# Performance work log

Hardware: AMD Instinct MI355X
Metric: run time of the kernel (lower is better)

## Reference

```python
import jax, jax.numpy as jnp
import numpy as np

N = 50000      # nodes
E = 800000     # edges (avg degree 16)
IN = 128       # input feature dim
HID = 32       # per-head hidden dim
H = 4          # attention heads
C = 40         # num classes
SLOPE = 0.2    # leaky relu negative slope


def setup_inputs() -> dict:
    key = jax.random.key(0)
    ks = jax.random.split(key, 14)
    s = 0.05
    inputs = jax.random.normal(ks[0], (N, IN), jnp.float32)
    target = jax.random.normal(ks[1], (N, IN), jnp.float32)
    lamb = jax.random.uniform(ks[2], (1,), jnp.float32)
    src = jax.random.randint(ks[3], (E,), 0, N, jnp.int32)
    dst = jax.random.randint(ks[4], (E,), 0, N, jnp.int32)
    W0 = jax.random.normal(ks[5], (IN, H * HID), jnp.float32) * s
    al0 = jax.random.normal(ks[6], (H, HID), jnp.float32) * s
    ar0 = jax.random.normal(ks[7], (H, HID), jnp.float32) * s
    W1 = jax.random.normal(ks[8], (H * HID, H * HID), jnp.float32) * s
    al1 = jax.random.normal(ks[9], (H, HID), jnp.float32) * s
    ar1 = jax.random.normal(ks[10], (H, HID), jnp.float32) * s
    Wout = jax.random.normal(ks[11], (H * HID, C), jnp.float32) * s
    bout = jnp.zeros((C,), jnp.float32)
    return dict(inputs=inputs, target=target, lamb=lamb,
                W0=W0, al0=al0, ar0=ar0, W1=W1, al1=al1, ar1=ar1,
                Wout=Wout, bout=bout, src=src, dst=dst)


def gat_conv(h, W, al, ar, src, dst, residual):
    # h: [N, in_dim]; W: [in_dim, H*HID]; al/ar: [H, HID]
    feat = (h @ W).reshape(N, H, HID)                  # [N,H,D]
    el = jnp.einsum('nhd,hd->nh', feat, al)            # [N,H]
    er = jnp.einsum('nhd,hd->nh', feat, ar)            # [N,H]
    e = jax.nn.leaky_relu(el[src] + er[dst], SLOPE)    # [E,H]
    # edge softmax over incoming edges of each dst node
    emax = jax.ops.segment_max(e, dst, num_segments=N)  # [N,H]
    ee = jnp.exp(e - emax[dst])                          # [E,H]
    denom = jax.ops.segment_sum(ee, dst, num_segments=N)
    a = ee / denom[dst]                                  # [E,H]
    msg = feat[src] * a[:, :, None]                      # [E,H,D]
    out = jax.ops.segment_sum(msg, dst, num_segments=N)  # [N,H,D]
    if residual:
        out = out + h.reshape(N, H, HID)  # identity residual (in == H*HID)
    return jax.nn.elu(out)


def reference(inputs, target, lamb, W0, al0, ar0, W1, al1, ar1, Wout, bout, src, dst):
    def path(x):
        h = gat_conv(x, W0, al0, ar0, src, dst, residual=False).reshape(N, H * HID)
        h = gat_conv(h, W1, al1, ar1, src, dst, residual=True).reshape(N, H * HID)
        return h

    h = path(inputs)
    h2 = path(target)
    lam = lamb[0]
    h = lam * h + (1.0 - lam) * h2   # mixup_hidden=True
    logits = h @ Wout + bout
    return (h, logits)
```

## Files before the change

### kernel.cpp

```cpp
#include <hip/hip_runtime.h>
#include <hip/hip_bf16.h>
#include <cstddef>

#define GN 50000
#define GE 800000
#define GH 4
#define GD 32
#define SLOPE 0.2f
#define LOG2E 1.4426950408889634f

typedef unsigned short ushort_t;
typedef unsigned int uint_t;
using short8 = __attribute__((ext_vector_type(8))) short;
using float4v = __attribute__((ext_vector_type(4))) float;

__device__ __forceinline__ ushort_t f2bf(float f) {
    union { float f; uint_t u; } v; v.f = f;
    uint_t r = v.u + 0x7fff + ((v.u >> 16) & 1);
    return (ushort_t)(r >> 16);
}
__device__ __forceinline__ float bflo(uint_t u) { return __uint_as_float(u << 16); }
__device__ __forceinline__ float bfhi(uint_t u) { return __uint_as_float(u & 0xffff0000u); }
__device__ __forceinline__ float bfu(ushort_t u) { return __uint_as_float((uint_t)u << 16); }

__device__ __forceinline__ uint_t cvt_pk_bf16(float lo, float hi) {
    uint_t r;
    asm("v_cvt_pk_bf16_f32 %0, %1, %2" : "=v"(r) : "v"(lo), "v"(hi));
    return r;
}

#if __has_builtin(__builtin_amdgcn_exp2f)
#define EXP2F(x) __builtin_amdgcn_exp2f(x)
#else
#define EXP2F(x) exp2f(x)
#endif

#define SWZ_B(v, imm) __uint_as_float((uint_t)__builtin_amdgcn_ds_swizzle((int)__float_as_uint(v), (imm)))

__device__ __forceinline__ int slotmap(int a) {
    return (a < GN) ? (a << 1) : (((a - GN) << 1) | 1);
}

#define NEXT 144
#define WSTRIDE (NEXT * 128)

__global__ __launch_bounds__(256) void k_cvt_hist(
    const float* __restrict__ W0, const float* __restrict__ W1,
    const float* __restrict__ Wout,
    const float* __restrict__ al0, const float* __restrict__ ar0,
    const float* __restrict__ al1, const float* __restrict__ ar1,
    ushort_t* __restrict__ wbt, ushort_t* __restrict__ woutb,
    const int* __restrict__ dst, int* __restrict__ deg, int* __restrict__ rank,
    int cvtb, int E) {
    if ((int)blockIdx.x >= cvtb) {
        int i = ((blockIdx.x - cvtb) * 256 + threadIdx.x) * 4;
        if (i + 3 < E) {
            int4 d = *(const int4*)&dst[i];
            rank[i + 0] = atomicAdd(&deg[d.x], 1);
            rank[i + 1] = atomicAdd(&deg[d.y], 1);
            rank[i + 2] = atomicAdd(&deg[d.z], 1);
            rank[i + 3] = atomicAdd(&deg[d.w], 1);
        } else {
            for (int k = i; k < E; k++) rank[k] = atomicAdd(&deg[dst[k]], 1);
        }
        return;
    }
    int t = blockIdx.x * 256 + threadIdx.x;
    if (t < 2 * WSTRIDE) {
        int m = t / WSTRIDE;
        int o = t % WSTRIDE;
        int n = o >> 7, k = o & 127;
        const float* W = m ? W1 : W0;
        float v;
        if (n < 128) {
            v = W[k * 128 + n];
        } else if (n < 136) {
            int j = n - 128;
            int h = j & 3;
            const float* a = (j < 4) ? (m ? al1 : al0) : (m ? ar1 : ar0);
            float s = 0.f;
#pragma unroll 8
            for (int d = 0; d < 32; d++) s += W[k * 128 + h * 32 + d] * a[h * 32 + d];
            v = s * LOG2E;
        } else {
            v = 0.f;
        }
        wbt[t] = f2bf(v);
    } else {
        int u = t - 2 * WSTRIDE;
        if (u < 48 * 128) {
            int n = u >> 7, k = u & 127;
            float w = (n < 40) ? Wout[k * 40 + n] : 0.f;
            ushort_t h = f2bf(w);
            woutb[u] = h;
            woutb[48 * 128 + u] = f2bf(w - bfu(h));
        }
    }
}

__global__ void k_scan1(const int* __restrict__ deg, int* __restrict__ row_ptr,
                        int* __restrict__ partials, int n) {
    __shared__ int s[256];
    int t = threadIdx.x;
    int i = blockIdx.x * 256 + t;
    int v = (i < n) ? deg[i] : 0;
    s[t] = v;
    __syncthreads();
    for (int off = 1; off < 256; off <<= 1) {
        int add = (t >= off) ? s[t - off] : 0;
        __syncthreads();
        s[t] += add;
        __syncthreads();
    }
    if (i < n) row_ptr[i] = s[t] - v;
    if (t == 255) partials[blockIdx.x] = s[255];
}

__global__ void k_scan2(int* __restrict__ partials, int nb) {
    __shared__ int s[256];
    int t = threadIdx.x;
    int v = (t < nb) ? partials[t] : 0;
    s[t] = v;
    __syncthreads();
    for (int off = 1; off < 256; off <<= 1) {
        int add = (t >= off) ? s[t - off] : 0;
        __syncthreads();
        s[t] += add;
        __syncthreads();
    }
    if (t < nb) partials[t] = s[t] - v;
}

__global__ void k_scan3(int* __restrict__ row_ptr,
                        const int* __restrict__ partials, int n, int E) {
    int i = blockIdx.x * 256 + threadIdx.x;
    if (i < n) {
        row_ptr[i] += partials[i >> 8];
        if (i == 0) row_ptr[n] = E;
    }
}

__global__ void k_fill(const int* __restrict__ src, const int* __restrict__ dst,
                       const int* __restrict__ rank, const int* __restrict__ row_ptr,
                       int* __restrict__ csr_src, int E) {
    int i = (blockIdx.x * 256 + threadIdx.x) * 4;
    if (i + 3 < E) {
        int4 d = *(const int4*)&dst[i];
        int4 s = *(const int4*)&src[i];
        int4 r = *(const int4*)&rank[i];
        csr_src[row_ptr[d.x] + r.x] = s.x;
        csr_src[row_ptr[d.y] + r.y] = s.y;
        csr_src[row_ptr[d.z] + r.z] = s.z;
        csr_src[row_ptr[d.w] + r.w] = s.w;
    } else {
        for (int k = i; k < E; k++)
            csr_src[row_ptr[dst[k]] + rank[k]] = src[k];
    }
}

__device__ __forceinline__ void store_c_ext(ushort_t* __restrict__ Cb,
                                            float* __restrict__ el,
                                            float* __restrict__ er,
                                            const float4v acc[2][9],
                                            int r0, int quad, int col, int M) {
#pragma unroll
    for (int rt = 0; rt < 2; rt++)
#pragma unroll
        for (int nt = 0; nt < 8; nt++) {
            int rb = r0 + rt * 16 + quad * 4;
            int c = nt * 16 + col;
            uint_t p01 = cvt_pk_bf16(acc[rt][nt][0], acc[rt][nt][1]);
            uint_t p23 = cvt_pk_bf16(acc[rt][nt][2], acc[rt][nt][3]);
            if (rb + 0 < M) Cb[(size_t)slotmap(rb + 0) * 128 + c] = (ushort_t)p01;
            if (rb + 1 < M) Cb[(size_t)slotmap(rb + 1) * 128 + c] = (ushort_t)(p01 >> 16);
            if (rb + 2 < M) Cb[(size_t)slotmap(rb + 2) * 128 + c] = (ushort_t)p23;
            if (rb + 3 < M) Cb[(size_t)slotmap(rb + 3) * 128 + c] = (ushort_t)(p23 >> 16);
        }
    if (col < 8) {
        float* dstp = (col < 4) ? el : er;
        int h = col & 3;
#pragma unroll
        for (int rt = 0; rt < 2; rt++)
#pragma unroll
            for (int r = 0; r < 4; r++) {
                int row = r0 + rt * 16 + quad * 4 + r;
                if (row < M) dstp[slotmap(row) * 4 + h] = acc[rt][8][r];
            }
    }
}

__global__ __launch_bounds__(256) void gemm_mfma32(const float* __restrict__ A0,
                                                   const float* __restrict__ A1,
                                                   const ushort_t* __restrict__ WbT,
                                                   ushort_t* __restrict__ Cb,
                                                   float* __restrict__ el,
                                                   float* __restrict__ er, int M) {
    __shared__ ushort_t Bs[NEXT][136];
    int tid = threadIdx.x;
    for (int i = tid; i < NEXT * 16; i += 256) {
        int n = i >> 4;
        int kc = (i & 15) << 3;
        *(short8*)&Bs[n][kc] = *(const short8*)&WbT[n * 128 + kc];
    }
    __syncthreads();
    int wid = tid >> 6, lane = tid & 63;
    int r0 = blockIdx.x * 128 + wid * 32;
    int col = lane & 15, quad = lane >> 4;
    float4v acc[2][9];
#pragma unroll
    for (int rt = 0; rt < 2; rt++)
#pragma unroll
        for (int t = 0; t < 9; t++) acc[rt][t] = (float4v){0.f, 0.f, 0.f, 0.f};
    int ar_[2] = {r0 + col, r0 + 16 + col};
    const float* Ap[2];
#pragma unroll
    for (int rt = 0; rt < 2; rt++) {
        int a = ar_[rt];
        Ap[rt] = (a < M) ? ((a < GN) ? (A0 + (size_t)a * 128)
                                     : (A1 + (size_t)(a - GN) * 128)) : nullptr;
    }
#pragma unroll
    for (int ks = 0; ks < 4; ks++) {
        short8 af[2];
#pragma unroll
        for (int rt = 0; rt < 2; rt++) {
            af[rt] = (short8){};
            if (Ap[rt]) {
                float4 v0 = *(const float4*)&Ap[rt][ks * 32 + quad * 8];
                float4 v1 = *(const float4*)&Ap[rt][ks * 32 + quad * 8 + 4];
                union { short8 s; uint_t u[4]; } cv;
                cv.u[0] = cvt_pk_bf16(v0.x, v0.y);
                cv.u[1] = cvt_pk_bf16(v0.z, v0.w);
                cv.u[2] = cvt_pk_bf16(v1.x, v1.y);
                cv.u[3] = cvt_pk_bf16(v1.z, v1.w);
                af[rt] = cv.s;
            }
        }
#pragma unroll
        for (int nt = 0; nt < 9; nt++) {
            short8 bf = *(const short8*)&Bs[nt * 16 + col][ks * 32 + quad * 8];
            acc[0][nt] = __builtin_amdgcn_mfma_f32_16x16x32_bf16(af[0], bf, acc[0][nt], 0, 0, 0);
            acc[1][nt] = __builtin_amdgcn_mfma_f32_16x16x32_bf16(af[1], bf, acc[1][nt], 0, 0, 0);
        }
    }
    store_c_ext(Cb, el, er, acc, r0, quad, col, M);
}

__global__ __launch_bounds__(256) void gemm_mfma(const ushort_t* __restrict__ A,
                                                 const ushort_t* __restrict__ WbT,
                                                 ushort_t* __restrict__ Cb,
                                                 float* __restrict__ el,
                                                 float* __restrict__ er, int M) {
    __shared__ ushort_t Bs[NEXT][136];
    int tid = threadIdx.x;
    for (int i = tid; i < NEXT * 16; i += 256) {
        int n = i >> 4;
        int kc = (i & 15) << 3;
        *(short8*)&Bs[n][kc] = *(const short8*)&WbT[n * 128 + kc];
    }
    __syncthreads();
    int wid = tid >> 6, lane = tid & 63;
    int r0 = blockIdx.x * 128 + wid * 32;
    int col = lane & 15, quad = lane >> 4;
    float4v acc[2][9];
#pragma unroll
    for (int rt = 0; rt < 2; rt++)
#pragma unroll
        for (int t = 0; t < 9; t++) acc[rt][t] = (float4v){0.f, 0.f, 0.f, 0.f};
    int ar_[2] = {r0 + col, r0 + 16 + col};
    const ushort_t* Ap[2];
#pragma unroll
    for (int rt = 0; rt < 2; rt++) {
        int a = ar_[rt];
        Ap[rt] = (a < M) ? (A + (size_t)slotmap(a) * 128) : nullptr;
    }
#pragma unroll
    for (int ks = 0; ks < 4; ks++) {
        short8 af[2];
#pragma unroll
        for (int rt = 0; rt < 2; rt++) {
            af[rt] = (short8){};
            if (Ap[rt]) af[rt] = *(const short8*)&Ap[rt][ks * 32 + quad * 8];
        }
#pragma unroll
        for (int nt = 0; nt < 9; nt++) {
            short8 bf = *(const short8*)&Bs[nt * 16 + col][ks * 32 + quad * 8];
            acc[0][nt] = __builtin_amdgcn_mfma_f32_16x16x32_bf16(af[0], bf, acc[0][nt], 0, 0, 0);
            acc[1][nt] = __builtin_amdgcn_mfma_f32_16x16x32_bf16(af[1], bf, acc[1][nt], 0, 0, 0);
        }
    }
    store_c_ext(Cb, el, er, acc, r0, quad, col, M);
}

__device__ __forceinline__ void agg_core(
    const ushort_t* __restrict__ featb, const float* __restrict__ el, float ern,
    const int* __restrict__ csr_src, int base, int deg, uint_t eo, uint_t fofs,
    int lk, float& v0, float& v1, float& v2, float& v3) {
    if (deg <= 0) { v0 = v1 = v2 = v3 = 0.f; return; }
    float a0 = 0.f, a1 = 0.f, a2 = 0.f, a3 = 0.f, ss = 0.f;
    int nblk = (deg + 15) >> 4;
    int e1 = base + deg - 1;
    int jb = base;
    int s[16], t[16];
#pragma unroll
    for (int k = 0; k < 16; k++) s[k] = csr_src[min(jb + k, e1)];
    float elA = el[(uint_t)csr_src[min(jb + lk, e1)] * 8u + eo];
    float elB = el[(uint_t)csr_src[min(jb + lk + 8, e1)] * 8u + eo];
    for (int b = 0;;) {
        int rem = deg - (b << 4);
        uint2 f[16];
#pragma unroll
        for (int k = 0; k < 16; k++)
            f[k] = *(const uint2*)&featb[(uint_t)s[k] * 256u + fofs];
        bool more = (b + 1) < nblk;
        float elA2 = 0.f, elB2 = 0.f;
        if (more) {
            int nj = jb + 16;
#pragma unroll
            for (int k = 0; k < 16; k++) t[k] = csr_src[min(nj + k, e1)];
            elA2 = el[(uint_t)csr_src[min(nj + lk, e1)] * 8u + eo];
            elB2 = el[(uint_t)csr_src[min(nj + lk + 8, e1)] * 8u + eo];
        }
        float eA = elA + ern; eA = fmaxf(eA, SLOPE * eA);
        float eB = elB + ern; eB = fmaxf(eB, SLOPE * eB);
        float wA = (lk < rem) ? EXP2F(eA) : 0.f;
        float wB = (lk + 8 < rem) ? EXP2F(eB) : 0.f;
        float wv[16];
        wv[0]  = SWZ_B(wA, 0x018); wv[1]  = SWZ_B(wA, 0x038);
        wv[2]  = SWZ_B(wA, 0x058); wv[3]  = SWZ_B(wA, 0x078);
        wv[4]  = SWZ_B(wA, 0x098); wv[5]  = SWZ_B(wA, 0x0B8);
        wv[6]  = SWZ_B(wA, 0x0D8); wv[7]  = SWZ_B(wA, 0x0F8);
        wv[8]  = SWZ_B(wB, 0x018); wv[9]  = SWZ_B(wB, 0x038);
        wv[10] = SWZ_B(wB, 0x058); wv[11] = SWZ_B(wB, 0x078);
        wv[12] = SWZ_B(wB, 0x098); wv[13] = SWZ_B(wB, 0x0B8);
        wv[14] = SWZ_B(wB, 0x0D8); wv[15] = SWZ_B(wB, 0x0F8);
#pragma unroll
        for (int k = 0; k < 16; k++) {
            float w = wv[k];
            ss += w;
            a0 += w * bflo(f[k].x);
            a1 += w * bfhi(f[k].x);
            a2 += w * bflo(f[k].y);
            a3 += w * bfhi(f[k].y);
        }
        if (!more) break;
        b++; jb += 16;
#pragma unroll
        for (int k = 0; k < 16; k++) s[k] = t[k];
        elA = elA2; elB = elB2;
    }
    float inv = 1.f / ss;
    v0 = a0 * inv; v1 = a1 * inv; v2 = a2 * inv; v3 = a3 * inv;
}

__global__ __launch_bounds__(512) void gat_agg_l1(
    const ushort_t* __restrict__ featb, const float* __restrict__ el,
    const float* __restrict__ er, const int* __restrict__ row_ptr,
    const int* __restrict__ csr_src, ushort_t* __restrict__ abuf) {
    int n = __builtin_amdgcn_readfirstlane(blockIdx.x * 8 + (threadIdx.x >> 6));
    if (n >= GN) return;
    int lane = threadIdx.x & 63;
    int half = lane >> 5;
    int q = lane & 31;
    int lk = lane & 7, q4 = q << 2;
    uint_t eo = (uint_t)(half * 4 + ((lane >> 3) & 3));
    uint_t fofs = (uint_t)(half * 128 + q4);
    float ern = er[(uint_t)n * 8u + eo];
    int base = row_ptr[n];
    int deg = row_ptr[n + 1] - base;
    float v0, v1, v2, v3;
    agg_core(featb, el, ern, csr_src, base, deg, eo, fofs, lk, v0, v1, v2, v3);
    v0 = v0 > 0.f ? v0 : __expf(v0) - 1.f;
    v1 = v1 > 0.f ? v1 : __expf(v1) - 1.f;
    v2 = v2 > 0.f ? v2 : __expf(v2) - 1.f;
    v3 = v3 > 0.f ? v3 : __expf(v3) - 1.f;
    size_t idx = ((size_t)(2 * n + half)) * 128 + q4;
    uint2 o;
    o.x = cvt_pk_bf16(v0, v1);
    o.y = cvt_pk_bf16(v2, v3);
    *(uint2*)&abuf[idx] = o;
}

__global__ __launch_bounds__(512) void gat_agg_l2(
    const ushort_t* __restrict__ featb, const float* __restrict__ el,
    const float* __restrict__ er, const int* __restrict__ row_ptr,
    const int* __restrict__ csr_src, const ushort_t* __restrict__ resid,
    const float* __restrict__ lamb, float* __restrict__ outh) {
    int tid = threadIdx.x;
    int n = __builtin_amdgcn_readfirstlane(blockIdx.x * 8 + (tid >> 6));
    if (n >= GN) return;
    int lane = tid & 63;
    int half = lane >> 5;
    int q = lane & 31;
    int lk = lane & 7, q4 = q << 2;
    uint_t eo = (uint_t)(half * 4 + ((lane >> 3) & 3));
    uint_t fofs = (uint_t)(half * 128 + q4);
    float ern = er[(uint_t)n * 8u + eo];
    int base = row_ptr[n];
    int deg = row_ptr[n + 1] - base;
    float v0, v1, v2, v3;
    agg_core(featb, el, ern, csr_src, base, deg, eo, fofs, lk, v0, v1, v2, v3);
    size_t idx = ((size_t)(2 * n + half)) * 128 + q4;
    ushort4 r = *(const ushort4*)&resid[idx];
    v0 += bfu(r.x); v1 += bfu(r.y); v2 += bfu(r.z); v3 += bfu(r.w);
    v0 = v0 > 0.f ? v0 : __expf(v0) - 1.f;
    v1 = v1 > 0.f ? v1 : __expf(v1) - 1.f;
    v2 = v2 > 0.f ? v2 : __expf(v2) - 1.f;
    v3 = v3 > 0.f ? v3 : __expf(v3) - 1.f;
    float p0 = __shfl_xor(v0, 32, 64);
    float p1 = __shfl_xor(v1, 32, 64);
    float p2 = __shfl_xor(v2, 32, 64);
    float p3 = __shfl_xor(v3, 32, 64);
    float lam = lamb[0];
    if (half == 0) {
        float m0 = lam * v0 + (1.f - lam) * p0;
        float m1 = lam * v1 + (1.f - lam) * p1;
        float m2 = lam * v2 + (1.f - lam) * p2;
        float m3 = lam * v3 + (1.f - lam) * p3;
        *(float4*)&outh[(size_t)n * 128 + q4] = make_float4(m0, m1, m2, m3);
    }
}

__global__ __launch_bounds__(256) void k_logits(const float* __restrict__ Hf,
                                                const ushort_t* __restrict__ Wb,
                                                const float* __restrict__ bout,
                                                float* __restrict__ outlog) {
    __shared__ ushort_t Bh[48][136];
    __shared__ ushort_t Bl[48][136];
    int tid = threadIdx.x;
    for (int i = tid; i < 48 * 16; i += 256) {
        int n = i >> 4;
        int kc = (i & 15) << 3;
        *(short8*)&Bh[n][kc] = *(const short8*)&Wb[n * 128 + kc];
        *(short8*)&Bl[n][kc] = *(const short8*)&Wb[48 * 128 + n * 128 + kc];
    }
    __syncthreads();
    int wid = tid >> 6, lane = tid & 63;
    int r0 = blockIdx.x * 128 + wid * 32;
    int col = lane & 15, quad = lane >> 4;
    float4v acc[2][3];
#pragma unroll
    for (int rt = 0; rt < 2; rt++)
#pragma unroll
        for (int nt = 0; nt < 3; nt++) acc[rt][nt] = (float4v){0.f, 0.f, 0.f, 0.f};
    int ar_[2] = {r0 + col, r0 + 16 + col};
#pragma unroll
    for (int ks = 0; ks < 4; ks++) {
        short8 ah[2], alo[2];
#pragma unroll
        for (int rt = 0; rt < 2; rt++) {
            ah[rt] = (short8){};
            alo[rt] = (short8){};
            if (ar_[rt] < GN) {
                const float* p = Hf + (size_t)ar_[rt] * 128 + ks * 32 + quad * 8;
                float4 x = *(const float4*)p;
                float4 y = *(const float4*)(p + 4);
                union { short8 s; uint_t u[4]; } ch, cl;
                ch.u[0] = cvt_pk_bf16(x.x, x.y);
                ch.u[1] = cvt_pk_bf16(x.z, x.w);
                ch.u[2] = cvt_pk_bf16(y.x, y.y);
                ch.u[3] = cvt_pk_bf16(y.z, y.w);
                cl.u[0] = cvt_pk_bf16(x.x - bflo(ch.u[0]), x.y - bfhi(ch.u[0]));
                cl.u[1] = cvt_pk_bf16(x.z - bflo(ch.u[1]), x.w - bfhi(ch.u[1]));
                cl.u[2] = cvt_pk_bf16(y.x - bflo(ch.u[2]), y.y - bfhi(ch.u[2]));
                cl.u[3] = cvt_pk_bf16(y.z - bflo(ch.u[3]), y.w - bfhi(ch.u[3]));
                ah[rt] = ch.s;
                alo[rt] = cl.s;
            }
        }
#pragma unroll
        for (int nt = 0; nt < 3; nt++) {
            short8 bh = *(const short8*)&Bh[nt * 16 + col][ks * 32 + quad * 8];
            short8 bl = *(const short8*)&Bl[nt * 16 + col][ks * 32 + quad * 8];
#pragma unroll
            for (int rt = 0; rt < 2; rt++) {
                acc[rt][nt] = __builtin_amdgcn_mfma_f32_16x16x32_bf16(ah[rt], bh, acc[rt][nt], 0, 0, 0);
                acc[rt][nt] = __builtin_amdgcn_mfma_f32_16x16x32_bf16(alo[rt], bh, acc[rt][nt], 0, 0, 0);
                acc[rt][nt] = __builtin_amdgcn_mfma_f32_16x16x32_bf16(ah[rt], bl, acc[rt][nt], 0, 0, 0);
            }
        }
    }
#pragma unroll
    for (int nt = 0; nt < 3; nt++) {
        int c = nt * 16 + col;
        if (c < 40) {
            float bv = bout[c];
#pragma unroll
            for (int rt = 0; rt < 2; rt++)
#pragma unroll
                for (int r = 0; r < 4; r++) {
                    int row = r0 + rt * 16 + quad * 4 + r;
                    if (row < GN) outlog[(size_t)row * 40 + c] = acc[rt][nt][r] + bv;
                }
        }
    }
}

extern "C" void kernel_launch(void* const* d_in, const int* in_sizes, int n_in,
                              void* d_out, int out_size, void* d_ws, size_t ws_size,
                              hipStream_t stream) {
    const float* inputs = (const float*)d_in[0];
    const float* target = (const float*)d_in[1];
    const float* lamb   = (const float*)d_in[2];
    const float* W0     = (const float*)d_in[3];
    const float* al0    = (const float*)d_in[4];
    const float* ar0    = (const float*)d_in[5];
    const float* W1     = (const float*)d_in[6];
    const float* al1    = (const float*)d_in[7];
    const float* ar1    = (const float*)d_in[8];
    const float* Wout   = (const float*)d_in[9];
    const float* bout   = (const float*)d_in[10];
    const int*   src    = (const int*)d_in[11];
    const int*   dst    = (const int*)d_in[12];

    float* out = (float*)d_out;
    float* outh = out;
    float* outlog = out + (size_t)GN * 128;

    const int NP = 2 * GN;
    ushort_t* featb = (ushort_t*)d_ws;
    ushort_t* abuf  = featb + (size_t)NP * 128;
    float* el = (float*)(abuf + (size_t)NP * 128);
    float* er = el + (size_t)NP * GH;
    ushort_t* wbt = (ushort_t*)(er + (size_t)NP * GH);
    int* row_ptr  = (int*)(wbt + 2 * WSTRIDE);
    int* wpos     = row_ptr + (GN + 1);
    int* csr_src  = wpos + GN;
    int* partials = csr_src + GE + 16;
    int* rank     = partials + 256;
    ushort_t* woutb = (ushort_t*)(rank + GE + 16);

    const int nb = (GN + 255) / 256;
    const int eb4 = (GE / 4 + 255) / 256;
    const int gblocks = (NP + 127) / 128;
    const int aggblocks = (GN + 7) / 8;
    const int lblocks = (GN + 127) / 128;
    const int cvtblocks = (2 * WSTRIDE + 48 * 128 + 255) / 256;

    hipMemsetAsync(wpos, 0, GN * sizeof(int), stream);
    k_cvt_hist<<<cvtblocks + eb4, 256, 0, stream>>>(W0, W1, Wout, al0, ar0, al1, ar1,
                                                    wbt, woutb, dst, wpos, rank,
                                                    cvtblocks, GE);

    k_scan1<<<nb, 256, 0, stream>>>(wpos, row_ptr, partials, GN);
    k_scan2<<<1, 256, 0, stream>>>(partials, nb);
    k_scan3<<<nb, 256, 0, stream>>>(row_ptr, partials, GN, GE);

    k_fill<<<eb4, 256, 0, stream>>>(src, dst, rank, row_ptr, csr_src, GE);

    gemm_mfma32<<<gblocks, 256, 0, stream>>>(inputs, target, wbt,
                                             featb, el, er, NP);
    gat_agg_l1<<<aggblocks, 512, 0, stream>>>(featb, el, er, row_ptr, csr_src, abuf);

    gemm_mfma<<<gblocks, 256, 0, stream>>>(abuf, wbt + WSTRIDE,
                                           featb, el, er, NP);
    gat_agg_l2<<<aggblocks, 512, 0, stream>>>(featb, el, er, row_ptr, csr_src,
                                              abuf, lamb, outh);

    k_logits<<<lblocks, 256, 0, stream>>>(outh, woutb, bout, outlog);
}
```

Measured before the change: 348.8 us.

## Fuse CSR build and weight conversion into one cooperative kernel with grid syncs

Replaces the memset, the histogram/convert kernel, the three scan kernels and the fill kernel with a single cooperative kernel of 512 blocks that uses grid-wide syncs between phases. The goal is to remove the launch overhead and inter-kernel gaps of six small launches. In exchange, each phase runs on a fixed 512-block grid with grid-stride loops, and the kernel now depends on cooperative-launch support and on all blocks being co-resident. Five grid syncs, each with its own cost, are added.

Result: slower. 625.3 us (+79.3%).

```diff
diff --git a/kernel.cpp b/kernel.cpp
--- a/kernel.cpp
+++ b/kernel.cpp
@@ -1,5 +1,6 @@
 #include <hip/hip_runtime.h>
 #include <hip/hip_bf16.h>
+#include <hip/hip_cooperative_groups.h>
 #include <cstddef>
 
 #define GN 50000
@@ -43,52 +44,49 @@
 
 #define NEXT 144
 #define WSTRIDE (NEXT * 128)
-
-__global__ __launch_bounds__(256) void k_cvt_hist(
+#define NB1 ((GN + 255) / 256)
+
+__global__ __launch_bounds__(256) void k_csr_coop(
     const float* __restrict__ W0, const float* __restrict__ W1,
     const float* __restrict__ Wout,
     const float* __restrict__ al0, const float* __restrict__ ar0,
     const float* __restrict__ al1, const float* __restrict__ ar1,
     ushort_t* __restrict__ wbt, ushort_t* __restrict__ woutb,
-    const int* __restrict__ dst, int* __restrict__ deg, int* __restrict__ rank,
-    int cvtb, int E) {
-    if ((int)blockIdx.x >= cvtb) {
-        int i = ((blockIdx.x - cvtb) * 256 + threadIdx.x) * 4;
-        if (i + 3 < E) {
-            int4 d = *(const int4*)&dst[i];
-            rank[i + 0] = atomicAdd(&deg[d.x], 1);
-            rank[i + 1] = atomicAdd(&deg[d.y], 1);
-            rank[i + 2] = atomicAdd(&deg[d.z], 1);
-            rank[i + 3] = atomicAdd(&deg[d.w], 1);
+    const int* __restrict__ src, const int* __restrict__ dst,
+    int* __restrict__ deg, int* __restrict__ rank,
+    int* __restrict__ row_ptr, int* __restrict__ partials,
+    int* __restrict__ csr_src) {
+    namespace cg = cooperative_groups;
+    cg::grid_group grid = cg::this_grid();
+    __shared__ int s[256];
+    const int T = gridDim.x * 256;
+    int gtid = blockIdx.x * 256 + threadIdx.x;
+
+    for (int t = gtid; t < GN; t += T) deg[t] = 0;
+    const int CVT = 2 * WSTRIDE + 48 * 128;
+    for (int t = gtid; t < CVT; t += T) {
+        if (t < 2 * WSTRIDE) {
+            int m = t / WSTRIDE;
+            int o = t % WSTRIDE;
+            int n = o >> 7, k = o & 127;
+            const float* W = m ? W1 : W0;
+            float v;
+            if (n < 128) {
+                v = W[k * 128 + n];
+            } else if (n < 136) {
+                int j = n - 128;
+                int h = j & 3;
+                const float* a = (j < 4) ? (m ? al1 : al0) : (m ? ar1 : ar0);
+                float sum = 0.f;
+#pragma unroll 8
+                for (int d = 0; d < 32; d++) sum += W[k * 128 + h * 32 + d] * a[h * 32 + d];
+                v = sum * LOG2E;
+            } else {
+                v = 0.f;
+            }
+            wbt[t] = f2bf(v);
         } else {
-            for (int k = i; k < E; k++) rank[k] = atomicAdd(&deg[dst[k]], 1);
-        }
-        return;
-    }
-    int t = blockIdx.x * 256 + threadIdx.x;
-    if (t < 2 * WSTRIDE) {
-        int m = t / WSTRIDE;
-        int o = t % WSTRIDE;
-        int n = o >> 7, k = o & 127;
-        const float* W = m ? W1 : W0;
-        float v;
-        if (n < 128) {
-            v = W[k * 128 + n];
-        } else if (n < 136) {
-            int j = n - 128;
-            int h = j & 3;
-            const float* a = (j < 4) ? (m ? al1 : al0) : (m ? ar1 : ar0);
-            float s = 0.f;
-#pragma unroll 8
-            for (int d = 0; d < 32; d++) s += W[k * 128 + h * 32 + d] * a[h * 32 + d];
-            v = s * LOG2E;
-        } else {
-            v = 0.f;
-        }
-        wbt[t] = f2bf(v);
-    } else {
-        int u = t - 2 * WSTRIDE;
-        if (u < 48 * 128) {
+            int u = t - 2 * WSTRIDE;
             int n = u >> 7, k = u & 127;
             float w = (n < 40) ? Wout[k * 40 + n] : 0.f;
             ushort_t h = f2bf(w);
@@ -96,65 +94,68 @@
             woutb[48 * 128 + u] = f2bf(w - bfu(h));
         }
     }
-}
-
-__global__ void k_scan1(const int* __restrict__ deg, int* __restrict__ row_ptr,
-                        int* __restrict__ partials, int n) {
-    __shared__ int s[256];
-    int t = threadIdx.x;
-    int i = blockIdx.x * 256 + t;
-    int v = (i < n) ? deg[i] : 0;
-    s[t] = v;
-    __syncthreads();
-    for (int off = 1; off < 256; off <<= 1) {
-        int add = (t >= off) ? s[t - off] : 0;
+    grid.sync();
+
+    for (int qi = gtid; qi < GE / 4; qi += T) {
+        int i = qi * 4;
+        int4 d = *(const int4*)&dst[i];
+        rank[i + 0] = atomicAdd(&deg[d.x], 1);
+        rank[i + 1] = atomicAdd(&deg[d.y], 1);
+        rank[i + 2] = atomicAdd(&deg[d.z], 1);
+        rank[i + 3] = atomicAdd(&deg[d.w], 1);
+    }
+    grid.sync();
+
+    if ((int)blockIdx.x < NB1) {
+        int t = threadIdx.x;
+        int i = blockIdx.x * 256 + t;
+        int v = (i < GN) ? deg[i] : 0;
+        s[t] = v;
         __syncthreads();
-        s[t] += add;
+        for (int off = 1; off < 256; off <<= 1) {
+            int add = (t >= off) ? s[t - off] : 0;
+            __syncthreads();
+            s[t] += add;
+            __syncthreads();
+        }
+        if (i < GN) row_ptr[i] = s[t] - v;
+        if (t == 255) partials[blockIdx.x] = s[255];
+    }
+    grid.sync();
+
+    if (blockIdx.x == 0) {
+        int t = threadIdx.x;
+        int v = (t < NB1) ? partials[t] : 0;
+        s[t] = v;
         __syncthreads();
-    }
-    if (i < n) row_ptr[i] = s[t] - v;
-    if (t == 255) partials[blockIdx.x] = s[255];
-}
-
-__global__ void k_scan2(int* __restrict__ partials, int nb) {
-    __shared__ int s[256];
-    int t = threadIdx.x;
-    int v = (t < nb) ? partials[t] : 0;
-    s[t] = v;
-    __syncthreads();
-    for (int off = 1; off < 256; off <<= 1) {
-        int add = (t >= off) ? s[t - off] : 0;
-        __syncthreads();
-        s[t] += add;
-        __syncthreads();
-    }
-    if (t < nb) partials[t] = s[t] - v;
-}
-
-__global__ void k_scan3(int* __restrict__ row_ptr,
-                        const int* __restrict__ partials, int n, int E) {
-    int i = blockIdx.x * 256 + threadIdx.x;
-    if (i < n) {
-        row_ptr[i] += partials[i >> 8];
-        if (i == 0) row_ptr[n] = E;
-    }
-}
-
-__global__ void k_fill(const int* __restrict__ src, const int* __restrict__ dst,
-                       const int* __restrict__ rank, const int* __restrict__ row_ptr,
-                       int* __restrict__ csr_src, int E) {
-    int i = (blockIdx.x * 256 + threadIdx.x) * 4;
-    if (i + 3 < E) {
+        for (int off = 1; off < 256; off <<= 1) {
+            int add = (t >= off) ? s[t - off] : 0;
+            __syncthreads();
+            s[t] += add;
+            __syncthreads();
+        }
+        if (t < NB1) partials[t] = s[t] - v;
+    }
+    grid.sync();
+
+    if ((int)blockIdx.x < NB1) {
+        int i = blockIdx.x * 256 + threadIdx.x;
+        if (i < GN) {
+            row_ptr[i] += partials[i >> 8];
+            if (i == 0) row_ptr[GN] = GE;
+        }
+    }
+    grid.sync();
+
+    for (int qi = gtid; qi < GE / 4; qi += T) {
+        int i = qi * 4;
         int4 d = *(const int4*)&dst[i];
-        int4 s = *(const int4*)&src[i];
+        int4 sv = *(const int4*)&src[i];
         int4 r = *(const int4*)&rank[i];
-        csr_src[row_ptr[d.x] + r.x] = s.x;
-        csr_src[row_ptr[d.y] + r.y] = s.y;
-        csr_src[row_ptr[d.z] + r.z] = s.z;
-        csr_src[row_ptr[d.w] + r.w] = s.w;
-    } else {
-        for (int k = i; k < E; k++)
-            csr_src[row_ptr[dst[k]] + rank[k]] = src[k];
+        csr_src[row_ptr[d.x] + r.x] = sv.x;
+        csr_src[row_ptr[d.y] + r.y] = sv.y;
+        csr_src[row_ptr[d.z] + r.z] = sv.z;
+        csr_src[row_ptr[d.w] + r.w] = sv.w;
     }
 }
 
@@ -530,23 +531,20 @@
     int* rank     = partials + 256;
     ushort_t* woutb = (ushort_t*)(rank + GE + 16);
 
-    const int nb = (GN + 255) / 256;
-    const int eb4 = (GE / 4 + 255) / 256;
     const int gblocks = (NP + 127) / 128;
     const int aggblocks = (GN + 7) / 8;
     const int lblocks = (GN + 127) / 128;
-    const int cvtblocks = (2 * WSTRIDE + 48 * 128 + 255) / 256;
-
-    hipMemsetAsync(wpos, 0, GN * sizeof(int), stream);
-    k_cvt_hist<<<cvtblocks + eb4, 256, 0, stream>>>(W0, W1, Wout, al0, ar0, al1, ar1,
-                                                    wbt, woutb, dst, wpos, rank,
-                                                    cvtblocks, GE);
-
-    k_scan1<<<nb, 256, 0, stream>>>(wpos, row_ptr, partials, GN);
-    k_scan2<<<1, 256, 0, stream>>>(partials, nb);
-    k_scan3<<<nb, 256, 0, stream>>>(row_ptr, partials, GN, GE);
-
-    k_fill<<<eb4, 256, 0, stream>>>(src, dst, rank, row_ptr, csr_src, GE);
+
+    {
+        void* args[] = {(void*)&W0, (void*)&W1, (void*)&Wout,
+                        (void*)&al0, (void*)&ar0, (void*)&al1, (void*)&ar1,
+                        (void*)&wbt, (void*)&woutb,
+                        (void*)&src, (void*)&dst,
+                        (void*)&wpos, (void*)&rank, (void*)&row_ptr,
+                        (void*)&partials, (void*)&csr_src};
+        hipLaunchCooperativeKernel((const void*)k_csr_coop, dim3(512), dim3(256),
+                                   args, 0, stream);
+    }
 
     gemm_mfma32<<<gblocks, 256, 0, stream>>>(inputs, target, wbt,
                                              featb, el, er, NP);
```
